# Performance work log

Measured on AMD Instinct MI355X. Metric: run time of the kernel, lower is better.

## Reference

```python
import jax, jax.numpy as jnp
import numpy as np

N, D, H, E, K = 8192, 2048, 2048, 8, 2
CAP = 4096  # per-expert capacity; avg load is N*K/E = 2048, so 4096 is >40 sigma safe for uniform routing


def setup_inputs() -> dict:
    key = jax.random.key(0)
    ks = jax.random.split(key, 6)
    x = jax.random.normal(ks[0], (N, D), dtype=jnp.float32)
    expert_weights = jax.random.uniform(ks[1], (N, K), dtype=jnp.float32)
    w1 = 0.02 * jax.random.normal(ks[2], (E, D, H), dtype=jnp.float32)
    w2 = 0.02 * jax.random.normal(ks[3], (E, H, D), dtype=jnp.float32)
    w3 = 0.02 * jax.random.normal(ks[4], (E, D, H), dtype=jnp.float32)
    expert_indices = jax.random.randint(ks[5], (N, K), 0, E, dtype=jnp.int32)
    batch_size_per_expert = jnp.bincount(expert_indices.reshape(-1), length=E).astype(jnp.int32)
    return {
        "x": x,
        "expert_weights": expert_weights,
        "w1": w1,
        "w2": w2,
        "w3": w3,
        "expert_indices": expert_indices,
        "batch_size_per_expert": batch_size_per_expert,
    }


def reference(x, expert_weights, w1, w2, w3, expert_indices, batch_size_per_expert):
    n, d = x.shape
    e = w1.shape[0]
    top_k = expert_indices.shape[-1]
    nt = n * top_k

    ei = expert_indices.reshape(-1).astype(jnp.int32)   # (NT,)
    ew = expert_weights.reshape(-1)                     # (NT,)

    # indices_and_bins: stable sort of expert ids + cumsum bins
    indices = jnp.argsort(ei)            # token-copy order grouped by expert (stable)
    bin_ids = ei[indices]                # (NT,) sorted expert ids
    bins = jnp.cumsum(batch_size_per_expert)
    starts = bins - batch_size_per_expert
    pos = jnp.arange(nt, dtype=jnp.int32) - starts[bin_ids]  # slot within expert bin

    # permute: gather tokens (indices // top_k maps copy -> source token)
    tok = indices // top_k
    x_perm = x[tok]                                     # (NT, D)

    # dispatch into (E, CAP, D) buffer
    buf = jnp.zeros((e, CAP, d), x.dtype).at[bin_ids, pos].set(x_perm)

    # per-expert SwiGLU MLP: (silu(x w1) * (x w3)) w2
    g = jax.nn.silu(jnp.einsum("ecd,edh->ech", buf, w1))
    u = jnp.einsum("ecd,edh->ech", buf, w3)
    out = jnp.einsum("ech,ehd->ecd", g * u, w2)         # (E, CAP, D)

    # unpermute + weighted combine (scatter-add over top_k copies)
    y_perm = out[bin_ids, pos]                          # (NT, D)
    w_perm = ew[indices]
    y = jnp.zeros_like(x).at[tok].add(y_perm * w_perm[:, None])
    return y
```

## Files before the change

kernel.cpp:

```cpp
#include <hip/hip_runtime.h>
#include <hip/hip_bf16.h>
#include <cstdio>
#include <cstdint>

#define N_TOK 8192
#define D_DIM 2048
#define H_DIM 2048
#define N_EXP 8
#define TOP_K 2
#define NT_CP (N_TOK * TOP_K)
#define BM 128
#define BN 128
#define BK 64
#define MT_MAX 32

typedef __attribute__((ext_vector_type(4))) float f32x4;
typedef __attribute__((ext_vector_type(8))) short s16x8;
typedef __attribute__((ext_vector_type(4))) short s16x4;

static constexpr size_t OFF_CNT  = 0;
static constexpr size_t OFF_ROWS = 256;
static constexpr size_t OFF_WTS  = OFF_ROWS + (size_t)(NT_CP + 128) * 4;
static constexpr size_t OFF_XB   = OFF_WTS  + (size_t)(NT_CP + 128) * 4;
static constexpr size_t OFF_ACT  = OFF_XB   + (size_t)N_TOK * D_DIM * 2;
static constexpr size_t OFF_W1T  = OFF_ACT  + (size_t)(NT_CP + 128) * H_DIM * 2;
static constexpr size_t OFF_W3T  = OFF_W1T  + (size_t)N_EXP * (size_t)H_DIM * D_DIM * 2;
static constexpr size_t OFF_W2T  = OFF_W3T  + (size_t)N_EXP * (size_t)H_DIM * D_DIM * 2;
static constexpr size_t WS_NEED  = OFF_W2T  + (size_t)N_EXP * (size_t)H_DIM * D_DIM * 2;

__device__ __forceinline__ short f2bf(float f) {
    uint32_t u = __builtin_bit_cast(uint32_t, f);
    uint32_t r = (u + 0x7FFFu + ((u >> 16) & 1u)) >> 16;
    return (short)r;
}

#define GLOAD_LDS16(g, l)                                                                  \
    __builtin_amdgcn_global_load_lds((const __attribute__((address_space(1))) void*)(g),   \
                                     (__attribute__((address_space(3))) void*)(l), 16, 0, 0)

__global__ void routing_kernel(const int* __restrict__ eidx, const float* __restrict__ ew,
                               const int* __restrict__ bspe, int* __restrict__ cnt,
                               int* __restrict__ rows, float* __restrict__ wts) {
    int i = blockIdx.x * blockDim.x + threadIdx.x;
    if (i >= NT_CP) return;
    int e = eidx[i];
    int off = 0;
#pragma unroll
    for (int j = 0; j < N_EXP; ++j) off += (j < e) ? bspe[j] : 0;
    int slot = atomicAdd(&cnt[e], 1);
    rows[off + slot] = i / TOP_K;
    wts[off + slot]  = ew[i];
}

__global__ void cast_x_kernel(const float* __restrict__ x, short* __restrict__ xb) {
    int i = blockIdx.x * blockDim.x + threadIdx.x;
    const int total = N_TOK * D_DIM / 4;
    if (i >= total) return;
    f32x4 v = ((const f32x4*)x)[i];
    s16x4 o;
    o.x = f2bf(v.x); o.y = f2bf(v.y); o.z = f2bf(v.z); o.w = f2bf(v.w);
    ((s16x4*)xb)[i] = o;
}

__global__ void transpose_cast_kernel(const float* __restrict__ in, short* __restrict__ out,
                                      int R, int C) {
    __shared__ float tile[32][33];
    int e = blockIdx.z;
    int c0 = blockIdx.x * 32, r0 = blockIdx.y * 32;
    const float* ine = in + (size_t)e * R * C;
    short* oute = out + (size_t)e * R * C;
    int tx = threadIdx.x, ty = threadIdx.y;
#pragma unroll
    for (int j = 0; j < 4; ++j)
        tile[ty + j * 8][tx] = ine[(size_t)(r0 + ty + j * 8) * C + c0 + tx];
    __syncthreads();
#pragma unroll
    for (int j = 0; j < 4; ++j)
        oute[(size_t)(c0 + ty + j * 8) * R + r0 + tx] = f2bf(tile[tx][ty + j * 8]);
}

__launch_bounds__(256, 2)
__global__ void gemm1_kernel(const short* __restrict__ xb, const short* __restrict__ w1t,
                             const short* __restrict__ w3t, const int* __restrict__ rows,
                             const int* __restrict__ bspe, short* __restrict__ act) {
    const int e = blockIdx.z;
    const int cnt_e = bspe[e];
    const int mt = blockIdx.y;
    if (mt * BM >= cnt_e) return;
    int off_e = 0;
#pragma unroll
    for (int j = 0; j < N_EXP; ++j) off_e += (j < e) ? bspe[j] : 0;
    const int p0 = off_e + mt * BM;
    const int bn0 = blockIdx.x * BN;
    int valid_rows = cnt_e - mt * BM;
    if (valid_rows > BM) valid_rows = BM;

    __shared__ short sA[BM * BK];
    __shared__ short sB1[BN * BK];
    __shared__ short sB3[BN * BK];

    const int tid = threadIdx.x;
    const int lane = tid & 63;
    const int wid = tid >> 6;

    const short* a_src[4];
#pragma unroll
    for (int i = 0; i < 4; ++i) {
        int r = i * 32 + (tid >> 3);
        int tok = (r < valid_rows) ? rows[p0 + r] : rows[p0];
        a_src[i] = xb + (size_t)tok * D_DIM + (tid & 7) * 8;
    }
    const short* b1_src = w1t + ((size_t)e * H_DIM + bn0 + (tid >> 3)) * D_DIM + (tid & 7) * 8;
    const short* b3_src = w3t + ((size_t)e * H_DIM + bn0 + (tid >> 3)) * D_DIM + (tid & 7) * 8;

    f32x4 acc1[4][4], acc3[4][4];
#pragma unroll
    for (int mi = 0; mi < 4; ++mi)
#pragma unroll
        for (int ni = 0; ni < 4; ++ni) {
            acc1[mi][ni] = (f32x4){0.f, 0.f, 0.f, 0.f};
            acc3[mi][ni] = (f32x4){0.f, 0.f, 0.f, 0.f};
        }

    const int wm = (wid >> 1) * 64;
    const int wn = (wid & 1) * 64;

    for (int k0 = 0; k0 < D_DIM; k0 += BK) {
#pragma unroll
        for (int i = 0; i < 4; ++i)
            GLOAD_LDS16(a_src[i] + k0, &sA[(i * 32 + wid * 8) * BK]);
#pragma unroll
        for (int i = 0; i < 4; ++i)
            GLOAD_LDS16(b1_src + (size_t)i * 32 * D_DIM + k0, &sB1[(i * 32 + wid * 8) * BK]);
#pragma unroll
        for (int i = 0; i < 4; ++i)
            GLOAD_LDS16(b3_src + (size_t)i * 32 * D_DIM + k0, &sB3[(i * 32 + wid * 8) * BK]);
        __syncthreads();
#pragma unroll
        for (int kk = 0; kk < 2; ++kk) {
            s16x8 af[4], b1f[4], b3f[4];
#pragma unroll
            for (int mi = 0; mi < 4; ++mi)
                af[mi] = *(const s16x8*)&sA[(wm + mi * 16 + (lane & 15)) * BK + kk * 32 + (lane >> 4) * 8];
#pragma unroll
            for (int ni = 0; ni < 4; ++ni) {
                b1f[ni] = *(const s16x8*)&sB1[(wn + ni * 16 + (lane & 15)) * BK + kk * 32 + (lane >> 4) * 8];
                b3f[ni] = *(const s16x8*)&sB3[(wn + ni * 16 + (lane & 15)) * BK + kk * 32 + (lane >> 4) * 8];
            }
#pragma unroll
            for (int mi = 0; mi < 4; ++mi)
#pragma unroll
                for (int ni = 0; ni < 4; ++ni) {
                    acc1[mi][ni] = __builtin_amdgcn_mfma_f32_16x16x32_bf16(af[mi], b1f[ni], acc1[mi][ni], 0, 0, 0);
                    acc3[mi][ni] = __builtin_amdgcn_mfma_f32_16x16x32_bf16(af[mi], b3f[ni], acc3[mi][ni], 0, 0, 0);
                }
        }
        __syncthreads();
    }

#pragma unroll
    for (int mi = 0; mi < 4; ++mi) {
#pragma unroll
        for (int j = 0; j < 4; ++j) {
            int row = wm + mi * 16 + (lane >> 4) * 4 + j;
            if (row < valid_rows) {
                size_t base = (size_t)(p0 + row) * H_DIM + bn0 + wn;
#pragma unroll
                for (int ni = 0; ni < 4; ++ni) {
                    float g = acc1[mi][ni][j];
                    float u = acc3[mi][ni][j];
                    float s = g / (1.0f + __expf(-g));
                    act[base + ni * 16 + (lane & 15)] = f2bf(s * u);
                }
            }
        }
    }
}

__launch_bounds__(256, 2)
__global__ void gemm2_kernel(const short* __restrict__ act, const short* __restrict__ w2t,
                             const int* __restrict__ rows, const float* __restrict__ wts,
                             const int* __restrict__ bspe, float* __restrict__ y) {
    const int e = blockIdx.z;
    const int cnt_e = bspe[e];
    const int mt = blockIdx.y;
    if (mt * BM >= cnt_e) return;
    int off_e = 0;
#pragma unroll
    for (int j = 0; j < N_EXP; ++j) off_e += (j < e) ? bspe[j] : 0;
    const int p0 = off_e + mt * BM;
    const int bn0 = blockIdx.x * BN;
    int valid_rows = cnt_e - mt * BM;
    if (valid_rows > BM) valid_rows = BM;

    __shared__ short sA[BM * BK];
    __shared__ short sB[BN * BK];

    const int tid = threadIdx.x;
    const int lane = tid & 63;
    const int wid = tid >> 6;

    const short* a_src = act + (size_t)(p0 + (tid >> 3)) * H_DIM + (tid & 7) * 8;
    const short* b_src = w2t + ((size_t)e * D_DIM + bn0 + (tid >> 3)) * H_DIM + (tid & 7) * 8;

    f32x4 acc[4][4];
#pragma unroll
    for (int mi = 0; mi < 4; ++mi)
#pragma unroll
        for (int ni = 0; ni < 4; ++ni) acc[mi][ni] = (f32x4){0.f, 0.f, 0.f, 0.f};

    const int wm = (wid >> 1) * 64;
    const int wn = (wid & 1) * 64;

    for (int k0 = 0; k0 < H_DIM; k0 += BK) {
#pragma unroll
        for (int i = 0; i < 4; ++i)
            GLOAD_LDS16(a_src + (size_t)i * 32 * H_DIM + k0, &sA[(i * 32 + wid * 8) * BK]);
#pragma unroll
        for (int i = 0; i < 4; ++i)
            GLOAD_LDS16(b_src + (size_t)i * 32 * H_DIM + k0, &sB[(i * 32 + wid * 8) * BK]);
        __syncthreads();
#pragma unroll
        for (int kk = 0; kk < 2; ++kk) {
            s16x8 af[4], bf[4];
#pragma unroll
            for (int mi = 0; mi < 4; ++mi)
                af[mi] = *(const s16x8*)&sA[(wm + mi * 16 + (lane & 15)) * BK + kk * 32 + (lane >> 4) * 8];
#pragma unroll
            for (int ni = 0; ni < 4; ++ni)
                bf[ni] = *(const s16x8*)&sB[(wn + ni * 16 + (lane & 15)) * BK + kk * 32 + (lane >> 4) * 8];
#pragma unroll
            for (int mi = 0; mi < 4; ++mi)
#pragma unroll
                for (int ni = 0; ni < 4; ++ni)
                    acc[mi][ni] = __builtin_amdgcn_mfma_f32_16x16x32_bf16(af[mi], bf[ni], acc[mi][ni], 0, 0, 0);
        }
        __syncthreads();
    }

#pragma unroll
    for (int mi = 0; mi < 4; ++mi) {
#pragma unroll
        for (int j = 0; j < 4; ++j) {
            int row = wm + mi * 16 + (lane >> 4) * 4 + j;
            if (row < valid_rows) {
                int p = p0 + row;
                int tok = rows[p];
                float w = wts[p];
                float* ybase = y + (size_t)tok * D_DIM + bn0 + wn + (lane & 15);
#pragma unroll
                for (int ni = 0; ni < 4; ++ni)
                    atomicAdd(ybase + ni * 16, acc[mi][ni][j] * w);
            }
        }
    }
}

extern "C" void kernel_launch(void* const* d_in, const int* in_sizes, int n_in,
                              void* d_out, int out_size, void* d_ws, size_t ws_size,
                              hipStream_t stream) {
    const float* x    = (const float*)d_in[0];
    const float* ew   = (const float*)d_in[1];
    const float* w1   = (const float*)d_in[2];
    const float* w2   = (const float*)d_in[3];
    const float* w3   = (const float*)d_in[4];
    const int* eidx   = (const int*)d_in[5];
    const int* bspe   = (const int*)d_in[6];
    float* y          = (float*)d_out;
    char* ws          = (char*)d_ws;

    if (ws_size < WS_NEED) {
        fprintf(stderr, "[kernel] ws too small: have %zu need %zu\n", ws_size, WS_NEED);
        return;
    }

    int*   cnt  = (int*)(ws + OFF_CNT);
    int*   rows = (int*)(ws + OFF_ROWS);
    float* wts  = (float*)(ws + OFF_WTS);
    short* xb   = (short*)(ws + OFF_XB);
    short* act  = (short*)(ws + OFF_ACT);
    short* w1t  = (short*)(ws + OFF_W1T);
    short* w3t  = (short*)(ws + OFF_W3T);
    short* w2t  = (short*)(ws + OFF_W2T);

    hipMemsetAsync(cnt, 0, 256, stream);
    hipMemsetAsync(y, 0, (size_t)N_TOK * D_DIM * 4, stream);

    routing_kernel<<<NT_CP / 256, 256, 0, stream>>>(eidx, ew, bspe, cnt, rows, wts);
    cast_x_kernel<<<(N_TOK * D_DIM / 4) / 256, 256, 0, stream>>>(x, xb);

    dim3 tgrid(H_DIM / 32, D_DIM / 32, N_EXP);
    transpose_cast_kernel<<<tgrid, dim3(32, 8), 0, stream>>>(w1, w1t, D_DIM, H_DIM);
    transpose_cast_kernel<<<tgrid, dim3(32, 8), 0, stream>>>(w3, w3t, D_DIM, H_DIM);
    transpose_cast_kernel<<<dim3(D_DIM / 32, H_DIM / 32, N_EXP), dim3(32, 8), 0, stream>>>(w2, w2t, H_DIM, D_DIM);

    gemm1_kernel<<<dim3(H_DIM / BN, MT_MAX, N_EXP), 256, 0, stream>>>(xb, w1t, w3t, rows, bspe, act);
    gemm2_kernel<<<dim3(D_DIM / BN, MT_MAX, N_EXP), 256, 0, stream>>>(act, w2t, rows, wts, bspe, y);
}
```

Measured before the change: 1.100 ms.

## Interleave w1/w3 into one weight matrix and fuse the three transpose kernels

New measurement: 1.072 ms. 2.6% less time.

```diff
diff --git a/kernel.cpp b/kernel.cpp
--- a/kernel.cpp
+++ b/kernel.cpp
@@ -23,9 +23,8 @@
 static constexpr size_t OFF_WTS  = OFF_ROWS + (size_t)(NT_CP + 128) * 4;
 static constexpr size_t OFF_XB   = OFF_WTS  + (size_t)(NT_CP + 128) * 4;
 static constexpr size_t OFF_ACT  = OFF_XB   + (size_t)N_TOK * D_DIM * 2;
-static constexpr size_t OFF_W1T  = OFF_ACT  + (size_t)(NT_CP + 128) * H_DIM * 2;
-static constexpr size_t OFF_W3T  = OFF_W1T  + (size_t)N_EXP * (size_t)H_DIM * D_DIM * 2;
-static constexpr size_t OFF_W2T  = OFF_W3T  + (size_t)N_EXP * (size_t)H_DIM * D_DIM * 2;
+static constexpr size_t OFF_W13T = OFF_ACT  + (size_t)(NT_CP + 128) * H_DIM * 2;
+static constexpr size_t OFF_W2T  = OFF_W13T + (size_t)N_EXP * 4096 * (size_t)D_DIM * 2;
 static constexpr size_t WS_NEED  = OFF_W2T  + (size_t)N_EXP * (size_t)H_DIM * D_DIM * 2;
 
 __device__ __forceinline__ short f2bf(float f) {
@@ -62,27 +61,42 @@
     ((s16x4*)xb)[i] = o;
 }
 
-__global__ void transpose_cast_kernel(const float* __restrict__ in, short* __restrict__ out,
-                                      int R, int C) {
-    __shared__ float tile[32][33];
-    int e = blockIdx.z;
-    int c0 = blockIdx.x * 32, r0 = blockIdx.y * 32;
-    const float* ine = in + (size_t)e * R * C;
-    short* oute = out + (size_t)e * R * C;
-    int tx = threadIdx.x, ty = threadIdx.y;
-#pragma unroll
-    for (int j = 0; j < 4; ++j)
-        tile[ty + j * 8][tx] = ine[(size_t)(r0 + ty + j * 8) * C + c0 + tx];
+__global__ void transpose_cast_fused(const float* __restrict__ w1, const float* __restrict__ w3,
+                                     const float* __restrict__ w2, short* __restrict__ w13t,
+                                     short* __restrict__ w2t) {
+    __shared__ float t[64][65];
+    const int slab = blockIdx.z;
+    const int mat = slab >> 3, e = slab & 7;
+    const float* in = (mat == 0 ? w1 : (mat == 1 ? w3 : w2)) + (size_t)e * D_DIM * H_DIM;
+    short* out = (mat == 2) ? (w2t + (size_t)e * D_DIM * H_DIM)
+                            : (w13t + (size_t)e * 4096 * D_DIM);
+    const int r0 = blockIdx.y * 64, c0 = blockIdx.x * 64;
+    const int tid = threadIdx.x;
+
+#pragma unroll
+    for (int p = 0; p < 4; ++p) {
+        int r = p * 16 + (tid >> 4);
+        int c4 = (tid & 15) * 4;
+        f32x4 v = *(const f32x4*)&in[(size_t)(r0 + r) * 2048 + c0 + c4];
+        t[r][c4 + 0] = v.x; t[r][c4 + 1] = v.y; t[r][c4 + 2] = v.z; t[r][c4 + 3] = v.w;
+    }
     __syncthreads();
 #pragma unroll
-    for (int j = 0; j < 4; ++j)
-        oute[(size_t)(c0 + ty + j * 8) * R + r0 + tx] = f2bf(tile[tx][ty + j * 8]);
+    for (int p = 0; p < 2; ++p) {
+        int c = c0 + p * 32 + (tid >> 3);
+        int r8 = (tid & 7) * 8;
+        s16x8 o;
+#pragma unroll
+        for (int j = 0; j < 8; ++j) o[j] = f2bf(t[r8 + j][c - c0]);
+        int row2 = (mat == 2) ? c : (((c >> 4) << 5) + ((mat == 1) ? 16 : 0) + (c & 15));
+        *(s16x8*)&out[(size_t)row2 * 2048 + r0 + r8] = o;
+    }
 }
 
 __launch_bounds__(256, 2)
-__global__ void gemm1_kernel(const short* __restrict__ xb, const short* __restrict__ w1t,
-                             const short* __restrict__ w3t, const int* __restrict__ rows,
-                             const int* __restrict__ bspe, short* __restrict__ act) {
+__global__ void gemm1_kernel(const short* __restrict__ xb, const short* __restrict__ w13t,
+                             const int* __restrict__ rows, const int* __restrict__ bspe,
+                             short* __restrict__ act) {
     const int e = blockIdx.z;
     const int cnt_e = bspe[e];
     const int mt = blockIdx.y;
@@ -96,8 +110,7 @@
     if (valid_rows > BM) valid_rows = BM;
 
     __shared__ short sA[BM * BK];
-    __shared__ short sB1[BN * BK];
-    __shared__ short sB3[BN * BK];
+    __shared__ short sB[BN * BK];
 
     const int tid = threadIdx.x;
     const int lane = tid & 63;
@@ -110,17 +123,13 @@
         int tok = (r < valid_rows) ? rows[p0 + r] : rows[p0];
         a_src[i] = xb + (size_t)tok * D_DIM + (tid & 7) * 8;
     }
-    const short* b1_src = w1t + ((size_t)e * H_DIM + bn0 + (tid >> 3)) * D_DIM + (tid & 7) * 8;
-    const short* b3_src = w3t + ((size_t)e * H_DIM + bn0 + (tid >> 3)) * D_DIM + (tid & 7) * 8;
-
-    f32x4 acc1[4][4], acc3[4][4];
+    const short* b_src = w13t + ((size_t)e * 4096 + bn0 + (tid >> 3)) * D_DIM + (tid & 7) * 8;
+
+    f32x4 acc[4][4];
 #pragma unroll
     for (int mi = 0; mi < 4; ++mi)
 #pragma unroll
-        for (int ni = 0; ni < 4; ++ni) {
-            acc1[mi][ni] = (f32x4){0.f, 0.f, 0.f, 0.f};
-            acc3[mi][ni] = (f32x4){0.f, 0.f, 0.f, 0.f};
-        }
+        for (int ni = 0; ni < 4; ++ni) acc[mi][ni] = (f32x4){0.f, 0.f, 0.f, 0.f};
 
     const int wm = (wid >> 1) * 64;
     const int wn = (wid & 1) * 64;
@@ -131,46 +140,40 @@
             GLOAD_LDS16(a_src[i] + k0, &sA[(i * 32 + wid * 8) * BK]);
 #pragma unroll
         for (int i = 0; i < 4; ++i)
-            GLOAD_LDS16(b1_src + (size_t)i * 32 * D_DIM + k0, &sB1[(i * 32 + wid * 8) * BK]);
-#pragma unroll
-        for (int i = 0; i < 4; ++i)
-            GLOAD_LDS16(b3_src + (size_t)i * 32 * D_DIM + k0, &sB3[(i * 32 + wid * 8) * BK]);
+            GLOAD_LDS16(b_src + (size_t)i * 32 * D_DIM + k0, &sB[(i * 32 + wid * 8) * BK]);
         __syncthreads();
 #pragma unroll
         for (int kk = 0; kk < 2; ++kk) {
-            s16x8 af[4], b1f[4], b3f[4];
+            s16x8 af[4], bf[4];
 #pragma unroll
             for (int mi = 0; mi < 4; ++mi)
                 af[mi] = *(const s16x8*)&sA[(wm + mi * 16 + (lane & 15)) * BK + kk * 32 + (lane >> 4) * 8];
 #pragma unroll
-            for (int ni = 0; ni < 4; ++ni) {
-                b1f[ni] = *(const s16x8*)&sB1[(wn + ni * 16 + (lane & 15)) * BK + kk * 32 + (lane >> 4) * 8];
-                b3f[ni] = *(const s16x8*)&sB3[(wn + ni * 16 + (lane & 15)) * BK + kk * 32 + (lane >> 4) * 8];
-            }
-#pragma unroll
-            for (int mi = 0; mi < 4; ++mi)
-#pragma unroll
-                for (int ni = 0; ni < 4; ++ni) {
-                    acc1[mi][ni] = __builtin_amdgcn_mfma_f32_16x16x32_bf16(af[mi], b1f[ni], acc1[mi][ni], 0, 0, 0);
-                    acc3[mi][ni] = __builtin_amdgcn_mfma_f32_16x16x32_bf16(af[mi], b3f[ni], acc3[mi][ni], 0, 0, 0);
-                }
-        }
-        __syncthreads();
-    }
-
+            for (int ni = 0; ni < 4; ++ni)
+                bf[ni] = *(const s16x8*)&sB[(wn + ni * 16 + (lane & 15)) * BK + kk * 32 + (lane >> 4) * 8];
+#pragma unroll
+            for (int mi = 0; mi < 4; ++mi)
+#pragma unroll
+                for (int ni = 0; ni < 4; ++ni)
+                    acc[mi][ni] = __builtin_amdgcn_mfma_f32_16x16x32_bf16(af[mi], bf[ni], acc[mi][ni], 0, 0, 0);
+        }
+        __syncthreads();
+    }
+
+    const int hbase = (bn0 + wn) >> 1;
 #pragma unroll
     for (int mi = 0; mi < 4; ++mi) {
 #pragma unroll
         for (int j = 0; j < 4; ++j) {
             int row = wm + mi * 16 + (lane >> 4) * 4 + j;
             if (row < valid_rows) {
-                size_t base = (size_t)(p0 + row) * H_DIM + bn0 + wn;
-#pragma unroll
-                for (int ni = 0; ni < 4; ++ni) {
-                    float g = acc1[mi][ni][j];
-                    float u = acc3[mi][ni][j];
+                size_t base = (size_t)(p0 + row) * H_DIM + hbase + (lane & 15);
+#pragma unroll
+                for (int p = 0; p < 2; ++p) {
+                    float g = acc[mi][2 * p][j];
+                    float u = acc[mi][2 * p + 1][j];
                     float s = g / (1.0f + __expf(-g));
-                    act[base + ni * 16 + (lane & 15)] = f2bf(s * u);
+                    act[base + p * 16] = f2bf(s * u);
                 }
             }
         }
@@ -279,8 +282,7 @@
     float* wts  = (float*)(ws + OFF_WTS);
     short* xb   = (short*)(ws + OFF_XB);
     short* act  = (short*)(ws + OFF_ACT);
-    short* w1t  = (short*)(ws + OFF_W1T);
-    short* w3t  = (short*)(ws + OFF_W3T);
+    short* w13t = (short*)(ws + OFF_W13T);
     short* w2t  = (short*)(ws + OFF_W2T);
 
     hipMemsetAsync(cnt, 0, 256, stream);
@@ -289,11 +291,8 @@
     routing_kernel<<<NT_CP / 256, 256, 0, stream>>>(eidx, ew, bspe, cnt, rows, wts);
     cast_x_kernel<<<(N_TOK * D_DIM / 4) / 256, 256, 0, stream>>>(x, xb);
 
-    dim3 tgrid(H_DIM / 32, D_DIM / 32, N_EXP);
-    transpose_cast_kernel<<<tgrid, dim3(32, 8), 0, stream>>>(w1, w1t, D_DIM, H_DIM);
-    transpose_cast_kernel<<<tgrid, dim3(32, 8), 0, stream>>>(w3, w3t, D_DIM, H_DIM);
-    transpose_cast_kernel<<<dim3(D_DIM / 32, H_DIM / 32, N_EXP), dim3(32, 8), 0, stream>>>(w2, w2t, H_DIM, D_DIM);
-
-    gemm1_kernel<<<dim3(H_DIM / BN, MT_MAX, N_EXP), 256, 0, stream>>>(xb, w1t, w3t, rows, bspe, act);
+    transpose_cast_fused<<<dim3(2048 / 64, 2048 / 64, 24), 256, 0, stream>>>(w1, w3, w2, w13t, w2t);
+
+    gemm1_kernel<<<dim3(4096 / BN, MT_MAX, N_EXP), 256, 0, stream>>>(xb, w13t, rows, bspe, act);
     gemm2_kernel<<<dim3(D_DIM / BN, MT_MAX, N_EXP), 256, 0, stream>>>(act, w2t, rows, wts, bspe, y);
 }
```
